# Optimization experiments

Hardware: AMD Instinct MI355X
Metric: run time of the kernel (lower is better)

The kernel has to match this reference:

```python
import jax, jax.numpy as jnp
import numpy as np

NOISE_STD = 0.1
TOP_K = 2

def setup_inputs() -> dict:
    key = jax.random.key(0)
    k1, k2, k3, k4 = jax.random.split(key, 4)
    B, S, H = 4, 4096, 2048
    E, SE, NS = 64, 64, 10
    x = jax.random.normal(k1, (B, S, H), dtype=jnp.float32)
    scale_embeddings = jax.random.normal(k2, (NS, SE), dtype=jnp.float32)
    # nn.Linear(H+SE, E, bias=False) weight: [E, H+SE]
    router_w = jax.random.normal(k3, (E, H + SE), dtype=jnp.float32) / np.sqrt(H + SE).astype(np.float32)
    # pre-sampled standard-normal noise (training path), scaled by NOISE_STD inside reference
    noise = jax.random.normal(k4, (B, S, E), dtype=jnp.float32)
    return {"x": x, "scale_embeddings": scale_embeddings, "router_w": router_w,
            "noise": noise, "scale_idx": 3}

def reference(x, scale_embeddings, router_w, noise, scale_idx):
    B, S, _ = x.shape
    # scale_idx is not None branch: lookup one scale embedding, broadcast over tokens
    emb = scale_embeddings[scale_idx]                      # [SE]
    emb = jnp.broadcast_to(emb, (B, S, emb.shape[-1]))     # [B,S,SE]
    x_with_scale = jnp.concatenate([x, emb], axis=-1)      # [B,S,H+SE]
    # router: bias-free linear projection to expert logits
    router_logits = jnp.einsum('bsd,ed->bse', x_with_scale, router_w)
    router_logits = router_logits + noise * NOISE_STD      # training noise injection
    routing_probs = jax.nn.softmax(router_logits, axis=-1)  # [B,S,E]
    routing_weights, selected_experts = jax.lax.top_k(routing_probs, TOP_K)
    routing_weights = routing_weights / routing_weights.sum(axis=-1, keepdims=True)
    # scatter normalized weights into dense dispatch tensor [B,S,E]
    dispatch = (jax.nn.one_hot(selected_experts, routing_probs.shape[-1],
                               dtype=routing_probs.dtype)
                * routing_weights[..., None]).sum(axis=-2)
    return dispatch
```

## Files before the change

### kernel.cpp

```cpp
#include <hip/hip_runtime.h>
#include <math.h>
#include <stdint.h>


#define H_DIM 2048
#define K_TOTAL 2112
#define E_DIM 64
#define SE_DIM 64
#define TPB 64
#define NBLOCKS 256
#define NKB 32
#define WP_TILE_BYTES 24576
#define WP_TOTAL (NKB * WP_TILE_BYTES)

typedef float  f32x4 __attribute__((ext_vector_type(4)));
typedef short  s16x8 __attribute__((ext_vector_type(8)));

typedef uint32_t __attribute__((address_space(1))) gu32_t;
typedef uint32_t __attribute__((address_space(3))) lu32_t;
__device__ __forceinline__ void gload_lds16(const void* g, void* l) {
    __builtin_amdgcn_global_load_lds((const gu32_t*)g, (lu32_t*)l, 16, 0, 0);
}

__device__ __forceinline__ unsigned short bf16_rne(float f) {
    uint32_t u = __float_as_uint(f);
    return (unsigned short)((u + 0x7FFFu + ((u >> 16) & 1u)) >> 16);
}
__device__ __forceinline__ float bf16_f32(unsigned short h) {
    return __uint_as_float(((uint32_t)h) << 16);
}

__global__ void prep_kernel(const float* __restrict__ W,
                            const float* __restrict__ se,
                            const int* __restrict__ sidx,
                            unsigned short* __restrict__ Wp,
                            float* __restrict__ tail) {
    if (blockIdx.x == 64) {
        int e = threadIdx.x;
        if (e < 64) {
            const float* emb = se + (*sidx) * SE_DIM;
            float t = 0.f;
            for (int j = 0; j < SE_DIM; ++j)
                t = fmaf(emb[j], W[(size_t)e * K_TOTAL + H_DIM + j], t);
            tail[e] = t;
        }
        return;
    }
    int item = blockIdx.x * 256 + threadIdx.x;
    int lane = item & 63;
    int nt   = (item >> 6) & 3;
    int s    = item >> 8;
    int e     = nt * 16 + (lane & 15);
    int kbase = s * 32 + (lane >> 4) * 8;
    const float* wr = W + (size_t)e * K_TOTAL + kbase;
    unsigned short p0[8], p1[8], p2[8];
    #pragma unroll
    for (int j = 0; j < 8; ++j) {
        float v = wr[j];
        unsigned short a0 = bf16_rne(v);
        float r1 = v - bf16_f32(a0);
        unsigned short a1 = bf16_rne(r1);
        float r2 = r1 - bf16_f32(a1);
        p0[j] = a0; p1[j] = a1; p2[j] = bf16_rne(r2);
    }
    size_t rec = ((size_t)s * 4 + nt) * 3;
    unsigned short* d0 = Wp + (rec + 0) * 512 + lane * 8;
    unsigned short* d1 = Wp + (rec + 1) * 512 + lane * 8;
    unsigned short* d2 = Wp + (rec + 2) * 512 + lane * 8;
    #pragma unroll
    for (int j = 0; j < 8; ++j) { d0[j] = p0[j]; d1[j] = p1[j]; d2[j] = p2[j]; }
}

#define SPLIT8(fa, fb, U0, U1, U2) {                                          \
    float rf[8] = {fa.x, fa.y, fa.z, fa.w, fb.x, fb.y, fb.z, fb.w};           \
    unsigned short q0[8], q1[8], q2[8];                                       \
    _Pragma("unroll")                                                         \
    for (int j = 0; j < 8; ++j) {                                             \
        float v = rf[j];                                                      \
        unsigned short a0 = bf16_rne(v);                                      \
        float r1 = v - bf16_f32(a0);                                          \
        unsigned short a1 = bf16_rne(r1);                                     \
        float r2 = r1 - bf16_f32(a1);                                         \
        q0[j] = a0; q1[j] = a1; q2[j] = bf16_rne(r2);                         \
    }                                                                         \
    U0 = make_uint4(q0[0]|((uint32_t)q0[1]<<16), q0[2]|((uint32_t)q0[3]<<16), \
                    q0[4]|((uint32_t)q0[5]<<16), q0[6]|((uint32_t)q0[7]<<16));\
    U1 = make_uint4(q1[0]|((uint32_t)q1[1]<<16), q1[2]|((uint32_t)q1[3]<<16), \
                    q1[4]|((uint32_t)q1[5]<<16), q1[6]|((uint32_t)q1[7]<<16));\
    U2 = make_uint4(q2[0]|((uint32_t)q2[1]<<16), q2[2]|((uint32_t)q2[3]<<16), \
                    q2[4]|((uint32_t)q2[5]<<16), q2[6]|((uint32_t)q2[7]<<16));\
}

#define CONVSTORE(buf) {                                                      \
    uint4 g0p0, g0p1, g0p2, g1p0, g1p1, g1p2;                                 \
    SPLIT8(xr0, xr1, g0p0, g0p1, g0p2);                                       \
    SPLIT8(xr2, xr3, g1p0, g1p1, g1p2);                                       \
    *(uint4*)&xp[buf][0][woff0] = g0p0;                                       \
    *(uint4*)&xp[buf][1][woff0] = g0p1;                                       \
    *(uint4*)&xp[buf][2][woff0] = g0p2;                                       \
    *(uint4*)&xp[buf][0][woff1] = g1p0;                                       \
    *(uint4*)&xp[buf][1][woff1] = g1p1;                                       \
    *(uint4*)&xp[buf][2][woff1] = g1p2;                                       \
}

__launch_bounds__(256)
__global__ void router_kernel(const float* __restrict__ x,
                              const unsigned char* __restrict__ Wp,
                              const float* __restrict__ tail_g,
                              const float* __restrict__ noise,
                              float* __restrict__ out) {
    __shared__ __align__(16) unsigned char xp[2][3][8192];
    __shared__ __align__(16) unsigned char wp[2][WP_TILE_BYTES];
    __shared__ float4 res[TPB];
    __shared__ float  tail_lds[E_DIM];

    const int tid  = threadIdx.x;
    const int lane = tid & 63;
    const int wave = __builtin_amdgcn_readfirstlane(tid >> 6);
    const int tok0 = blockIdx.x * TPB;

    const int st = tid >> 2, su = tid & 3;
    const float* xrow = x + (size_t)(tok0 + st) * H_DIM + su * 16;
    const int woff0 = st * 128 + (((su * 2)     ^ (st & 7)) << 4);
    const int woff1 = st * 128 + (((su * 2 + 1) ^ (st & 7)) << 4);

    const int arow = wave * 16 + (lane & 15);
    const int aq = lane >> 4, as = lane & 7;
    const int aoff0 = arow * 128 + ((aq ^ as) << 4);
    const int aoff1 = arow * 128 + (((4 + aq) ^ as) << 4);
    const int blane = lane * 16;

    if (tid < 64) tail_lds[tid] = tail_g[tid];

    #pragma unroll
    for (int i = 0; i < 6; ++i)
        gload_lds16(Wp + (size_t)(tid + i * 256) * 16, &wp[0][(tid + i * 256) * 16]);
    float4 xr0 = *(const float4*)(xrow + 0);
    float4 xr1 = *(const float4*)(xrow + 4);
    float4 xr2 = *(const float4*)(xrow + 8);
    float4 xr3 = *(const float4*)(xrow + 12);
    CONVSTORE(0);
    xr0 = *(const float4*)(xrow + 64 + 0);
    xr1 = *(const float4*)(xrow + 64 + 4);
    xr2 = *(const float4*)(xrow + 64 + 8);
    xr3 = *(const float4*)(xrow + 64 + 12);

    f32x4 acc0 = {0.f, 0.f, 0.f, 0.f}, acc1 = acc0, acc2 = acc0, acc3 = acc0;

    for (int kb = 0; kb < NKB; ++kb) {
        __syncthreads();
        const int cbuf = kb & 1, nbuf = cbuf ^ 1;
        if (kb + 1 < NKB) {
            #pragma unroll
            for (int i = 0; i < 6; ++i)
                gload_lds16(Wp + (size_t)(kb + 1) * WP_TILE_BYTES + (tid + i * 256) * 16,
                            &wp[nbuf][(tid + i * 256) * 16]);
            CONVSTORE(nbuf);
        }
        if (kb + 2 < NKB) {
            const float* p = xrow + (size_t)(kb + 2) * 64;
            xr0 = *(const float4*)(p + 0);
            xr1 = *(const float4*)(p + 4);
            xr2 = *(const float4*)(p + 8);
            xr3 = *(const float4*)(p + 12);
        } else if (kb == NKB - 1) {
            #pragma unroll
            for (int i = 0; i < 4; ++i)
                gload_lds16(noise + (size_t)tok0 * 64 + (size_t)(tid + i * 256) * 4,
                            &xp[0][0][(tid + i * 256) * 16]);
        }

        const unsigned char* xpb = &xp[cbuf][0][0];
        const unsigned char* wb  = &wp[cbuf][0];
        #pragma unroll
        for (int s2 = 0; s2 < 2; ++s2) {
            const int aoff = s2 ? aoff1 : aoff0;
            s16x8 A0 = *(const s16x8*)&xpb[0 * 8192 + aoff];
            s16x8 A1 = *(const s16x8*)&xpb[1 * 8192 + aoff];
            s16x8 A2 = *(const s16x8*)&xpb[2 * 8192 + aoff];
            #pragma unroll
            for (int nt = 0; nt < 4; ++nt) {
                const int rb = ((s2 * 4 + nt) * 3) * 1024 + blane;
                s16x8 B0 = *(const s16x8*)&wb[rb];
                s16x8 B1 = *(const s16x8*)&wb[rb + 1024];
                s16x8 B2 = *(const s16x8*)&wb[rb + 2048];
                f32x4 a = (nt == 0) ? acc0 : (nt == 1) ? acc1 : (nt == 2) ? acc2 : acc3;
                a = __builtin_amdgcn_mfma_f32_16x16x32_bf16(A0, B0, a, 0, 0, 0);
                a = __builtin_amdgcn_mfma_f32_16x16x32_bf16(A0, B1, a, 0, 0, 0);
                a = __builtin_amdgcn_mfma_f32_16x16x32_bf16(A1, B0, a, 0, 0, 0);
                a = __builtin_amdgcn_mfma_f32_16x16x32_bf16(A0, B2, a, 0, 0, 0);
                a = __builtin_amdgcn_mfma_f32_16x16x32_bf16(A1, B1, a, 0, 0, 0);
                a = __builtin_amdgcn_mfma_f32_16x16x32_bf16(A2, B0, a, 0, 0, 0);
                if (nt == 0) acc0 = a; else if (nt == 1) acc1 = a;
                else if (nt == 2) acc2 = a; else acc3 = a;
            }
        }
    }

    __syncthreads();
    const float* nz = (const float*)&xp[0][0][0];
    const int c = lane & 15;

    #pragma unroll
    for (int r = 0; r < 4; ++r) {
        const int tloc = wave * 16 + aq * 4 + r;
        float v0 = acc0[r] + tail_lds[c]      + 0.1f * nz[tloc * 64 + c];
        float v1 = acc1[r] + tail_lds[c + 16] + 0.1f * nz[tloc * 64 + c + 16];
        float v2 = acc2[r] + tail_lds[c + 32] + 0.1f * nz[tloc * 64 + c + 32];
        float v3 = acc3[r] + tail_lds[c + 48] + 0.1f * nz[tloc * 64 + c + 48];
        float V1 = v0; int I1 = c;
        float V2 = -__builtin_inff(); int I2 = c;
        if (v1 > V1) { V2 = V1; I2 = I1; V1 = v1; I1 = c + 16; }
        else if (v1 > V2) { V2 = v1; I2 = c + 16; }
        if (v2 > V1) { V2 = V1; I2 = I1; V1 = v2; I1 = c + 32; }
        else if (v2 > V2) { V2 = v2; I2 = c + 32; }
        if (v3 > V1) { V2 = V1; I2 = I1; V1 = v3; I1 = c + 48; }
        else if (v3 > V2) { V2 = v3; I2 = c + 48; }
        #pragma unroll
        for (int m = 8; m; m >>= 1) {
            float o1 = __shfl_xor(V1, m, 64); int oi1 = __shfl_xor(I1, m, 64);
            float o2 = __shfl_xor(V2, m, 64); int oi2 = __shfl_xor(I2, m, 64);
            if (o1 > V1 || (o1 == V1 && oi1 < I1)) {
                float nv2; int ni2;
                if (V1 > o2 || (V1 == o2 && I1 < oi2)) { nv2 = V1; ni2 = I1; }
                else                                   { nv2 = o2; ni2 = oi2; }
                V1 = o1; I1 = oi1; V2 = nv2; I2 = ni2;
            } else {
                if (o1 > V2 || (o1 == V2 && oi1 < I2)) { V2 = o1; I2 = oi1; }
            }
        }
        if (c == r) {
            float d   = expf(V2 - V1);
            float inv = 1.0f / (1.0f + d);
            res[tloc] = make_float4(inv, __int_as_float(I1), d * inv, __int_as_float(I2));
        }
    }
    __syncthreads();

    float4* outb = (float4*)out + (size_t)blockIdx.x * (TPB * E_DIM / 4);
    #pragma unroll
    for (int pp = 0; pp < 4; ++pp) {
        int p = tid + pp * 256;
        int t = p >> 4, cc = p & 15;
        float4 rr = res[t];
        int ri1 = __float_as_int(rr.y), ri2 = __float_as_int(rr.w);
        int e = cc * 4;
        float4 o;
        o.x = (e + 0 == ri1) ? rr.x : (e + 0 == ri2) ? rr.z : 0.0f;
        o.y = (e + 1 == ri1) ? rr.x : (e + 1 == ri2) ? rr.z : 0.0f;
        o.z = (e + 2 == ri1) ? rr.x : (e + 2 == ri2) ? rr.z : 0.0f;
        o.w = (e + 3 == ri1) ? rr.x : (e + 3 == ri2) ? rr.z : 0.0f;
        outb[p] = o;
    }
}

extern "C" void kernel_launch(void* const* d_in, const int* in_sizes, int n_in,
                              void* d_out, int out_size, void* d_ws, size_t ws_size,
                              hipStream_t stream) {
    const float* x     = (const float*)d_in[0];
    const float* se    = (const float*)d_in[1];
    const float* W     = (const float*)d_in[2];
    const float* noise = (const float*)d_in[3];
    const int*   sidx  = (const int*)d_in[4];
    float* out = (float*)d_out;

    unsigned short* Wp   = (unsigned short*)d_ws;
    float*          tail = (float*)((char*)d_ws + WP_TOTAL);

    hipLaunchKernelGGL(prep_kernel, dim3(65), dim3(256), 0, stream, W, se, sidx, Wp, tail);
    hipLaunchKernelGGL(router_kernel, dim3(NBLOCKS), dim3(256), 0, stream,
                       x, (const unsigned char*)Wp, tail, noise, out);
}
```

Baseline: 239.2 us.

## Drop LDS staging; load x and packed weights straight into registers per wave

The router kernel no longer stages x and the split-bf16 weights through double-buffered LDS with block-wide barriers. Each wave now loads its own x fragment and the B-operand weight fragments directly from global memory into registers, prefetching one k-step ahead. The three-way bf16 split of x uses packed float2-to-bf162 conversion, and noise is read directly from global memory. This removes barriers and LDS traffic, but every wave re-reads the full weight matrix from global/L2 and register pressure rises, which is why occupancy is pinned to one block.

```diff
diff --git a/kernel.cpp b/kernel.cpp
--- a/kernel.cpp
+++ b/kernel.cpp
@@ -1,4 +1,5 @@
 #include <hip/hip_runtime.h>
+#include <hip/hip_bf16.h>
 #include <math.h>
 #include <stdint.h>
 
@@ -9,18 +10,12 @@
 #define SE_DIM 64
 #define TPB 64
 #define NBLOCKS 256
-#define NKB 32
-#define WP_TILE_BYTES 24576
-#define WP_TOTAL (NKB * WP_TILE_BYTES)
+#define NSTEP 64
+#define WP_TOTAL (NSTEP * 12 * 1024)
 
 typedef float  f32x4 __attribute__((ext_vector_type(4)));
 typedef short  s16x8 __attribute__((ext_vector_type(8)));
-
-typedef uint32_t __attribute__((address_space(1))) gu32_t;
-typedef uint32_t __attribute__((address_space(3))) lu32_t;
-__device__ __forceinline__ void gload_lds16(const void* g, void* l) {
-    __builtin_amdgcn_global_load_lds((const gu32_t*)g, (lu32_t*)l, 16, 0, 0);
-}
+typedef unsigned int u32x4 __attribute__((ext_vector_type(4)));
 
 __device__ __forceinline__ unsigned short bf16_rne(float f) {
     uint32_t u = __float_as_uint(f);
@@ -28,6 +23,9 @@
 }
 __device__ __forceinline__ float bf16_f32(unsigned short h) {
     return __uint_as_float(((uint32_t)h) << 16);
+}
+__device__ __forceinline__ uint32_t bits_of_bf2(__hip_bfloat162 h) {
+    uint32_t u; __builtin_memcpy(&u, &h, 4); return u;
 }
 
 __global__ void prep_kernel(const float* __restrict__ W,
@@ -63,7 +61,7 @@
         float r2 = r1 - bf16_f32(a1);
         p0[j] = a0; p1[j] = a1; p2[j] = bf16_rne(r2);
     }
-    size_t rec = ((size_t)s * 4 + nt) * 3;
+    size_t rec = (size_t)s * 12 + nt * 3;
     unsigned short* d0 = Wp + (rec + 0) * 512 + lane * 8;
     unsigned short* d1 = Wp + (rec + 1) * 512 + lane * 8;
     unsigned short* d2 = Wp + (rec + 2) * 512 + lane * 8;
@@ -71,143 +69,102 @@
     for (int j = 0; j < 8; ++j) { d0[j] = p0[j]; d1[j] = p1[j]; d2[j] = p2[j]; }
 }
 
-#define SPLIT8(fa, fb, U0, U1, U2) {                                          \
-    float rf[8] = {fa.x, fa.y, fa.z, fa.w, fb.x, fb.y, fb.z, fb.w};           \
-    unsigned short q0[8], q1[8], q2[8];                                       \
-    _Pragma("unroll")                                                         \
-    for (int j = 0; j < 8; ++j) {                                             \
-        float v = rf[j];                                                      \
-        unsigned short a0 = bf16_rne(v);                                      \
-        float r1 = v - bf16_f32(a0);                                          \
-        unsigned short a1 = bf16_rne(r1);                                     \
-        float r2 = r1 - bf16_f32(a1);                                         \
-        q0[j] = a0; q1[j] = a1; q2[j] = bf16_rne(r2);                         \
-    }                                                                         \
-    U0 = make_uint4(q0[0]|((uint32_t)q0[1]<<16), q0[2]|((uint32_t)q0[3]<<16), \
-                    q0[4]|((uint32_t)q0[5]<<16), q0[6]|((uint32_t)q0[7]<<16));\
-    U1 = make_uint4(q1[0]|((uint32_t)q1[1]<<16), q1[2]|((uint32_t)q1[3]<<16), \
-                    q1[4]|((uint32_t)q1[5]<<16), q1[6]|((uint32_t)q1[7]<<16));\
-    U2 = make_uint4(q2[0]|((uint32_t)q2[1]<<16), q2[2]|((uint32_t)q2[3]<<16), \
-                    q2[4]|((uint32_t)q2[5]<<16), q2[6]|((uint32_t)q2[7]<<16));\
-}
-
-#define CONVSTORE(buf) {                                                      \
-    uint4 g0p0, g0p1, g0p2, g1p0, g1p1, g1p2;                                 \
-    SPLIT8(xr0, xr1, g0p0, g0p1, g0p2);                                       \
-    SPLIT8(xr2, xr3, g1p0, g1p1, g1p2);                                       \
-    *(uint4*)&xp[buf][0][woff0] = g0p0;                                       \
-    *(uint4*)&xp[buf][1][woff0] = g0p1;                                       \
-    *(uint4*)&xp[buf][2][woff0] = g0p2;                                       \
-    *(uint4*)&xp[buf][0][woff1] = g1p0;                                       \
-    *(uint4*)&xp[buf][1][woff1] = g1p1;                                       \
-    *(uint4*)&xp[buf][2][woff1] = g1p2;                                       \
-}
-
-__launch_bounds__(256)
+__device__ __forceinline__ void split3(const float4 fa, const float4 fb,
+                                       s16x8& P0, s16x8& P1, s16x8& P2) {
+    float f[8] = {fa.x, fa.y, fa.z, fa.w, fb.x, fb.y, fb.z, fb.w};
+    uint32_t d0[4], d1[4], d2[4];
+    #pragma unroll
+    for (int p = 0; p < 4; ++p) {
+        float v0 = f[2 * p], v1 = f[2 * p + 1];
+        uint32_t u0 = bits_of_bf2(__float22bfloat162_rn(make_float2(v0, v1)));
+        float r0 = v0 - __uint_as_float(u0 << 16);
+        float r1 = v1 - __uint_as_float(u0 & 0xffff0000u);
+        uint32_t u1 = bits_of_bf2(__float22bfloat162_rn(make_float2(r0, r1)));
+        float s0 = r0 - __uint_as_float(u1 << 16);
+        float s1 = r1 - __uint_as_float(u1 & 0xffff0000u);
+        uint32_t u2 = bits_of_bf2(__float22bfloat162_rn(make_float2(s0, s1)));
+        d0[p] = u0; d1[p] = u1; d2[p] = u2;
+    }
+    u32x4 q0 = {d0[0], d0[1], d0[2], d0[3]};
+    u32x4 q1 = {d1[0], d1[1], d1[2], d1[3]};
+    u32x4 q2 = {d2[0], d2[1], d2[2], d2[3]};
+    __builtin_memcpy(&P0, &q0, 16);
+    __builtin_memcpy(&P1, &q1, 16);
+    __builtin_memcpy(&P2, &q2, 16);
+}
+
+__launch_bounds__(256, 1)
 __global__ void router_kernel(const float* __restrict__ x,
-                              const unsigned char* __restrict__ Wp,
+                              const uint4* __restrict__ wp4,
                               const float* __restrict__ tail_g,
                               const float* __restrict__ noise,
                               float* __restrict__ out) {
-    __shared__ __align__(16) unsigned char xp[2][3][8192];
-    __shared__ __align__(16) unsigned char wp[2][WP_TILE_BYTES];
     __shared__ float4 res[TPB];
-    __shared__ float  tail_lds[E_DIM];
 
     const int tid  = threadIdx.x;
     const int lane = tid & 63;
     const int wave = __builtin_amdgcn_readfirstlane(tid >> 6);
     const int tok0 = blockIdx.x * TPB;
-
-    const int st = tid >> 2, su = tid & 3;
-    const float* xrow = x + (size_t)(tok0 + st) * H_DIM + su * 16;
-    const int woff0 = st * 128 + (((su * 2)     ^ (st & 7)) << 4);
-    const int woff1 = st * 128 + (((su * 2 + 1) ^ (st & 7)) << 4);
-
-    const int arow = wave * 16 + (lane & 15);
-    const int aq = lane >> 4, as = lane & 7;
-    const int aoff0 = arow * 128 + ((aq ^ as) << 4);
-    const int aoff1 = arow * 128 + (((4 + aq) ^ as) << 4);
-    const int blane = lane * 16;
-
-    if (tid < 64) tail_lds[tid] = tail_g[tid];
-
-    #pragma unroll
-    for (int i = 0; i < 6; ++i)
-        gload_lds16(Wp + (size_t)(tid + i * 256) * 16, &wp[0][(tid + i * 256) * 16]);
-    float4 xr0 = *(const float4*)(xrow + 0);
-    float4 xr1 = *(const float4*)(xrow + 4);
-    float4 xr2 = *(const float4*)(xrow + 8);
-    float4 xr3 = *(const float4*)(xrow + 12);
-    CONVSTORE(0);
-    xr0 = *(const float4*)(xrow + 64 + 0);
-    xr1 = *(const float4*)(xrow + 64 + 4);
-    xr2 = *(const float4*)(xrow + 64 + 8);
-    xr3 = *(const float4*)(xrow + 64 + 12);
-
-    f32x4 acc0 = {0.f, 0.f, 0.f, 0.f}, acc1 = acc0, acc2 = acc0, acc3 = acc0;
-
-    for (int kb = 0; kb < NKB; ++kb) {
-        __syncthreads();
-        const int cbuf = kb & 1, nbuf = cbuf ^ 1;
-        if (kb + 1 < NKB) {
+    const int row  = lane & 15;
+    const int quad = lane >> 4;
+    const int c    = row;
+
+    const float* aptr = x + (size_t)(tok0 + wave * 16 + row) * H_DIM + quad * 8;
+
+    f32x4 acc[4];
+    #pragma unroll
+    for (int nt = 0; nt < 4; ++nt) acc[nt] = (f32x4){0.f, 0.f, 0.f, 0.f};
+
+    float4 arA = *(const float4*)(aptr);
+    float4 arB = *(const float4*)(aptr + 4);
+    uint4 bcur[12];
+    #pragma unroll
+    for (int q = 0; q < 12; ++q) bcur[q] = wp4[(size_t)q * 64 + lane];
+
+    #pragma unroll 2
+    for (int s = 0; s < NSTEP; ++s) {
+        float4 nrA, nrB;
+        uint4 bnxt[12];
+        if (s + 1 < NSTEP) {
+            const float* ap = aptr + (size_t)(s + 1) * 32;
+            nrA = *(const float4*)(ap);
+            nrB = *(const float4*)(ap + 4);
             #pragma unroll
-            for (int i = 0; i < 6; ++i)
-                gload_lds16(Wp + (size_t)(kb + 1) * WP_TILE_BYTES + (tid + i * 256) * 16,
-                            &wp[nbuf][(tid + i * 256) * 16]);
-            CONVSTORE(nbuf);
-        }
-        if (kb + 2 < NKB) {
-            const float* p = xrow + (size_t)(kb + 2) * 64;
-            xr0 = *(const float4*)(p + 0);
-            xr1 = *(const float4*)(p + 4);
-            xr2 = *(const float4*)(p + 8);
-            xr3 = *(const float4*)(p + 12);
-        } else if (kb == NKB - 1) {
-            #pragma unroll
-            for (int i = 0; i < 4; ++i)
-                gload_lds16(noise + (size_t)tok0 * 64 + (size_t)(tid + i * 256) * 4,
-                            &xp[0][0][(tid + i * 256) * 16]);
-        }
-
-        const unsigned char* xpb = &xp[cbuf][0][0];
-        const unsigned char* wb  = &wp[cbuf][0];
+            for (int q = 0; q < 12; ++q)
+                bnxt[q] = wp4[((size_t)(s + 1) * 12 + q) * 64 + lane];
+        }
+        s16x8 A0, A1, A2;
+        split3(arA, arB, A0, A1, A2);
         #pragma unroll
-        for (int s2 = 0; s2 < 2; ++s2) {
-            const int aoff = s2 ? aoff1 : aoff0;
-            s16x8 A0 = *(const s16x8*)&xpb[0 * 8192 + aoff];
-            s16x8 A1 = *(const s16x8*)&xpb[1 * 8192 + aoff];
-            s16x8 A2 = *(const s16x8*)&xpb[2 * 8192 + aoff];
-            #pragma unroll
-            for (int nt = 0; nt < 4; ++nt) {
-                const int rb = ((s2 * 4 + nt) * 3) * 1024 + blane;
-                s16x8 B0 = *(const s16x8*)&wb[rb];
-                s16x8 B1 = *(const s16x8*)&wb[rb + 1024];
-                s16x8 B2 = *(const s16x8*)&wb[rb + 2048];
-                f32x4 a = (nt == 0) ? acc0 : (nt == 1) ? acc1 : (nt == 2) ? acc2 : acc3;
-                a = __builtin_amdgcn_mfma_f32_16x16x32_bf16(A0, B0, a, 0, 0, 0);
-                a = __builtin_amdgcn_mfma_f32_16x16x32_bf16(A0, B1, a, 0, 0, 0);
-                a = __builtin_amdgcn_mfma_f32_16x16x32_bf16(A1, B0, a, 0, 0, 0);
-                a = __builtin_amdgcn_mfma_f32_16x16x32_bf16(A0, B2, a, 0, 0, 0);
-                a = __builtin_amdgcn_mfma_f32_16x16x32_bf16(A1, B1, a, 0, 0, 0);
-                a = __builtin_amdgcn_mfma_f32_16x16x32_bf16(A2, B0, a, 0, 0, 0);
-                if (nt == 0) acc0 = a; else if (nt == 1) acc1 = a;
-                else if (nt == 2) acc2 = a; else acc3 = a;
-            }
-        }
-    }
-
-    __syncthreads();
-    const float* nz = (const float*)&xp[0][0][0];
-    const int c = lane & 15;
-
+        for (int nt = 0; nt < 4; ++nt) {
+            s16x8 B0, B1, B2;
+            __builtin_memcpy(&B0, &bcur[nt * 3 + 0], 16);
+            __builtin_memcpy(&B1, &bcur[nt * 3 + 1], 16);
+            __builtin_memcpy(&B2, &bcur[nt * 3 + 2], 16);
+            f32x4 a = acc[nt];
+            a = __builtin_amdgcn_mfma_f32_16x16x32_bf16(A0, B0, a, 0, 0, 0);
+            a = __builtin_amdgcn_mfma_f32_16x16x32_bf16(A0, B1, a, 0, 0, 0);
+            a = __builtin_amdgcn_mfma_f32_16x16x32_bf16(A1, B0, a, 0, 0, 0);
+            a = __builtin_amdgcn_mfma_f32_16x16x32_bf16(A0, B2, a, 0, 0, 0);
+            a = __builtin_amdgcn_mfma_f32_16x16x32_bf16(A1, B1, a, 0, 0, 0);
+            a = __builtin_amdgcn_mfma_f32_16x16x32_bf16(A2, B0, a, 0, 0, 0);
+            acc[nt] = a;
+        }
+        arA = nrA; arB = nrB;
+        #pragma unroll
+        for (int q = 0; q < 12; ++q) bcur[q] = bnxt[q];
+    }
+
+    float tl0 = tail_g[c],      tl1 = tail_g[c + 16];
+    float tl2 = tail_g[c + 32], tl3 = tail_g[c + 48];
     #pragma unroll
     for (int r = 0; r < 4; ++r) {
-        const int tloc = wave * 16 + aq * 4 + r;
-        float v0 = acc0[r] + tail_lds[c]      + 0.1f * nz[tloc * 64 + c];
-        float v1 = acc1[r] + tail_lds[c + 16] + 0.1f * nz[tloc * 64 + c + 16];
-        float v2 = acc2[r] + tail_lds[c + 32] + 0.1f * nz[tloc * 64 + c + 32];
-        float v3 = acc3[r] + tail_lds[c + 48] + 0.1f * nz[tloc * 64 + c + 48];
+        const int tloc = wave * 16 + quad * 4 + r;
+        const float* nz = noise + (size_t)(tok0 + tloc) * E_DIM;
+        float v0 = acc[0][r] + tl0 + 0.1f * nz[c];
+        float v1 = acc[1][r] + tl1 + 0.1f * nz[c + 16];
+        float v2 = acc[2][r] + tl2 + 0.1f * nz[c + 32];
+        float v3 = acc[3][r] + tl3 + 0.1f * nz[c + 48];
         float V1 = v0; int I1 = c;
         float V2 = -__builtin_inff(); int I2 = c;
         if (v1 > V1) { V2 = V1; I2 = I1; V1 = v1; I1 = c + 16; }
@@ -269,5 +226,5 @@
 
     hipLaunchKernelGGL(prep_kernel, dim3(65), dim3(256), 0, stream, W, se, sidx, Wp, tail);
     hipLaunchKernelGGL(router_kernel, dim3(NBLOCKS), dim3(256), 0, stream,
-                       x, (const unsigned char*)Wp, tail, noise, out);
-}
+                       x, (const uint4*)Wp, tail, noise, out);
+}
```

New measurement: 239.2 us. About the same (-0.0%).
